# Kernel optimization log

Measured on AMD Instinct MI355X. Metric: run time of the kernel, lower is better.

The kernel has to match this reference:

```python
import jax, jax.numpy as jnp
import numpy as np

N_FACES = 40000
N_EDGES = 60000
NNZ = 3 * N_FACES  # 3 boundary edges per triangular face
IN_CH = 512
MID_CH = 512
OUT_CH = 512


def setup_inputs() -> dict:
    key = jax.random.key(0)
    k1, k2, k3 = jax.random.split(key, 3)
    x = jax.random.normal(k1, (N_FACES, IN_CH), dtype=jnp.float32)
    # xavier-uniform-ish scale with gain 1.414 as in TopoModelX Conv.reset_parameters
    W1 = jax.random.normal(k2, (IN_CH, MID_CH), dtype=jnp.float32) * (1.414 / np.sqrt(IN_CH))
    W2 = jax.random.normal(k3, (MID_CH, OUT_CH), dtype=jnp.float32) * (1.414 / np.sqrt(MID_CH))
    # COO incidence B2 [n_edges, n_faces]: face f -> edges (3f)%E,(3f+1)%E,(3f+2)%E
    i = jnp.arange(NNZ)
    face_idx = (i // 3).astype(jnp.int32)
    edge_idx = (i % N_EDGES).astype(jnp.int32)
    vals = jnp.ones((NNZ,), dtype=jnp.float32)
    return {"x": x, "W1": W1, "W2": W2, "edge_idx": edge_idx, "face_idx": face_idx, "vals": vals}


def _spmm(rows, cols, vals, x, n_rows):
    # y[r, :] = sum_{nnz with row r} vals * x[col, :]
    return jax.ops.segment_sum(vals[:, None] * x[cols], rows, num_segments=n_rows)


def reference(x, W1, W2, edge_idx, face_idx, vals):
    # row sums of B2 and B2^T for aggr_norm
    deg_e = jax.ops.segment_sum(vals, edge_idx, num_segments=N_EDGES)  # [n_edges]
    deg_f = jax.ops.segment_sum(vals, face_idx, num_segments=N_FACES)  # [n_faces]
    # conv level1: faces -> edges
    h = _spmm(edge_idx, face_idx, vals, x @ W1, N_EDGES)  # [n_edges, mid]
    h = jax.nn.sigmoid(h / deg_e[:, None])
    # conv level2: edges -> faces (transpose incidence)
    y = _spmm(face_idx, edge_idx, vals, h @ W2, N_FACES)  # [n_faces, out]
    return jax.nn.sigmoid(y / deg_f[:, None])
```

## Files before the change

### kernel.cpp

```cpp
#include <hip/hip_runtime.h>
#include <cstdint>

#define N_FACES_C 40000
#define N_EDGES_C 60000
#define CH        512

typedef __bf16 bf16_t;
typedef __bf16 bf16x8 __attribute__((ext_vector_type(8)));
typedef float  f32x4  __attribute__((ext_vector_type(4)));
static_assert(sizeof(bf16x8) == 16, "bf16x8 must be 16B");

__global__ void detect_dtype(const unsigned int* __restrict__ vals_bits, int* __restrict__ flag) {
  if (blockIdx.x == 0 && threadIdx.x == 0)
    *flag = (vals_bits[0] == 0x3F803F80u) ? 1 : 0;
}

__device__ __forceinline__ float load_val(const void* vals, int i, bool isbf16) {
  return isbf16 ? (float)((const bf16_t*)vals)[i] : ((const float*)vals)[i];
}

__device__ __forceinline__ float fast_sigmoid(float z) {
  float e = __builtin_amdgcn_exp2f(z * -1.44269504f);
  return __builtin_amdgcn_rcpf(1.0f + e);
}

__global__ void count_deg_kernel(const int* __restrict__ ei, const int* __restrict__ fi,
                                 const void* __restrict__ vals, int nnz,
                                 float* __restrict__ deg_e, float* __restrict__ deg_f,
                                 int* __restrict__ cnt_e, int* __restrict__ cnt_f,
                                 const int* __restrict__ flag) {
  int i = blockIdx.x * 256 + threadIdx.x;
  if (i >= nnz) return;
  bool isb = (*flag != 0);
  float v = load_val(vals, i, isb);
  int e = ei[i], f = fi[i];
  atomicAdd(&deg_e[e], v);
  atomicAdd(&deg_f[f], v);
  atomicAdd(&cnt_e[e], 1);
  atomicAdd(&cnt_f[f], 1);
}

__global__ void scan_part2(const int* __restrict__ cntE, int nE, int* __restrict__ bsumE,
                           const int* __restrict__ cntF, int nF, int* __restrict__ bsumF,
                           int nbE) {
  __shared__ int wsum[4];
  int bx = blockIdx.x;
  const int* cnt; int n; int* bsum; int b;
  if (bx < nbE) { cnt = cntE; n = nE; bsum = bsumE; b = bx; }
  else          { cnt = cntF; n = nF; bsum = bsumF; b = bx - nbE; }
  int t = threadIdx.x;
  int lane = t & 63, wave = t >> 6;
  int base = b * 1024 + t * 4;
  int s = 0;
#pragma unroll
  for (int k = 0; k < 4; ++k) {
    int idx = base + k;
    if (idx < n) s += cnt[idx];
  }
#pragma unroll
  for (int o = 32; o > 0; o >>= 1) s += __shfl_down(s, o);
  if (lane == 0) wsum[wave] = s;
  __syncthreads();
  if (t == 0) bsum[b] = wsum[0] + wsum[1] + wsum[2] + wsum[3];
}

__global__ void scan_bsums2(int* __restrict__ bsumE, int nbE, int* __restrict__ bsumF, int nbF) {
  int wave = threadIdx.x >> 6;
  int lane = threadIdx.x & 63;
  int* bsum = wave ? bsumF : bsumE;
  int nb    = wave ? nbF   : nbE;
  int orig = (lane < nb) ? bsum[lane] : 0;
  int v = orig;
#pragma unroll
  for (int o = 1; o < 64; o <<= 1) {
    int u = __shfl_up(v, o);
    if (lane >= o) v += u;
  }
  if (lane < nb) bsum[lane] = v - orig;
}

__global__ void scan_final2(const int* __restrict__ cntE, int nE, const int* __restrict__ bsumE,
                            int* __restrict__ ptrE, int* __restrict__ curE,
                            const int* __restrict__ cntF, int nF, const int* __restrict__ bsumF,
                            int* __restrict__ ptrF, int* __restrict__ curF, int nbE) {
  __shared__ int wsum[4];
  int bx = blockIdx.x;
  const int* cnt; int n; const int* bsum; int* ptr; int* cur; int b;
  if (bx < nbE) { cnt = cntE; n = nE; bsum = bsumE; ptr = ptrE; cur = curE; b = bx; }
  else          { cnt = cntF; n = nF; bsum = bsumF; ptr = ptrF; cur = curF; b = bx - nbE; }
  int t = threadIdx.x;
  int lane = t & 63, wave = t >> 6;
  int base = b * 1024 + t * 4;
  int c[4];
  int s = 0;
#pragma unroll
  for (int k = 0; k < 4; ++k) {
    int idx = base + k;
    c[k] = (idx < n) ? cnt[idx] : 0;
    s += c[k];
  }
  int v = s;
#pragma unroll
  for (int o = 1; o < 64; o <<= 1) {
    int u = __shfl_up(v, o);
    if (lane >= o) v += u;
  }
  if (lane == 63) wsum[wave] = v;
  __syncthreads();
  int woff = 0;
  for (int w = 0; w < wave; ++w) woff += wsum[w];
  int run = bsum[b] + woff + (v - s);
#pragma unroll
  for (int k = 0; k < 4; ++k) {
    int idx = base + k;
    if (idx < n) {
      ptr[idx] = run;
      cur[idx] = run;
      run += c[k];
      if (idx == n - 1) ptr[n] = run;
    }
  }
}

__global__ void csr_fill(const int* __restrict__ ei, const int* __restrict__ fi,
                         const void* __restrict__ vals, int nnz,
                         int* __restrict__ cur_e, int* __restrict__ col_e, float* __restrict__ val_e,
                         int* __restrict__ cur_f, int* __restrict__ col_f, float* __restrict__ val_f,
                         const int* __restrict__ flag) {
  int i = blockIdx.x * 256 + threadIdx.x;
  if (i >= nnz) return;
  bool isb = (*flag != 0);
  int e = ei[i], f = fi[i];
  float v = load_val(vals, i, isb);
  int p = atomicAdd(&cur_e[e], 1);
  col_e[p] = f; val_e[p] = v;
  int q = atomicAdd(&cur_f[f], 1);
  col_f[q] = e; val_f[q] = v;
}

__global__ void transposeW2(const void* __restrict__ W1, bf16_t* __restrict__ W1t,
                            const void* __restrict__ W2, bf16_t* __restrict__ W2t,
                            const int* __restrict__ flag) {
  __shared__ bf16_t tile[32][33];
  bool isb = (*flag != 0);
  const void* W = blockIdx.z ? W2 : W1;
  bf16_t*    Wt = blockIdx.z ? W2t : W1t;
  int bx = blockIdx.x * 32, by = blockIdx.y * 32;
  int tx = threadIdx.x, ty = threadIdx.y;
#pragma unroll
  for (int r = 0; r < 32; r += 8) {
    size_t idx = (size_t)(by + ty + r) * CH + bx + tx;
    tile[ty + r][tx] = isb ? ((const bf16_t*)W)[idx] : (bf16_t)((const float*)W)[idx];
  }
  __syncthreads();
#pragma unroll
  for (int r = 0; r < 32; r += 8)
    Wt[(size_t)(bx + ty + r) * CH + by + tx] = tile[tx][ty + r];
}

__global__ void spmm_div(const int* __restrict__ ptr, const int* __restrict__ cols,
                         const float* __restrict__ vals, const void* __restrict__ X,
                         const float* __restrict__ deg, bf16_t* __restrict__ Y,
                         int nRows, int nCols, int nnz,
                         const int* __restrict__ flag, int force_bf16) {
  int row = blockIdx.x * 4 + (threadIdx.x >> 6);
  if (row >= nRows) return;
  bool xb = force_bf16 || (*flag != 0);
  int lane = threadIdx.x & 63;
  int beg = ptr[row], end = ptr[row + 1];
  if (beg < 0) beg = 0;
  if (end > nnz) end = nnz;
  float acc[8];
#pragma unroll
  for (int t = 0; t < 8; ++t) acc[t] = 0.f;
  const int lofs = lane * 8;
  if (xb) {
    const bf16_t* Xb = (const bf16_t*)X;
    for (int p = beg; p < end; ++p) {
      int c = cols[p];
      if ((unsigned)c >= (unsigned)nCols) c = 0;
      float v = vals[p];
      bf16x8 xv = *(const bf16x8*)(Xb + (size_t)c * CH + lofs);
#pragma unroll
      for (int t = 0; t < 8; ++t) acc[t] += v * (float)xv[t];
    }
  } else {
    const float* Xf = (const float*)X;
    for (int p = beg; p < end; ++p) {
      int c = cols[p];
      if ((unsigned)c >= (unsigned)nCols) c = 0;
      float v = vals[p];
      const float* src = Xf + (size_t)c * CH + lofs;
      float4 a = *(const float4*)src;
      float4 b = *(const float4*)(src + 4);
      acc[0] += v * a.x; acc[1] += v * a.y; acc[2] += v * a.z; acc[3] += v * a.w;
      acc[4] += v * b.x; acc[5] += v * b.y; acc[6] += v * b.z; acc[7] += v * b.w;
    }
  }
  float d = deg[row];
  float invd = (d != 0.f) ? (1.0f / d) : 0.f;
  bf16x8 o;
#pragma unroll
  for (int t = 0; t < 8; ++t) o[t] = (bf16_t)(acc[t] * invd);
  *(bf16x8*)(Y + (size_t)row * CH + lofs) = o;
}

__global__ __launch_bounds__(256)
void gemm_sig(const bf16_t* __restrict__ A, const bf16_t* __restrict__ Bt,
              void* __restrict__ C, int M, int N, int K,
              const int* __restrict__ flag, int final_out) {
  __shared__ __align__(16) bf16_t As[128 * 64];
  __shared__ __align__(16) bf16_t Bs[128 * 64];
  const int tid  = threadIdx.x;
  const int lane = tid & 63;
  const int wave = tid >> 6;
  const int r0 = blockIdx.y * 128;
  const int c0 = blockIdx.x * 128;
  const int wr = (wave >> 1) * 64;
  const int wc = (wave & 1) * 64;
  const int q   = lane >> 4;
  const int l16 = lane & 15;
  const int srow_base = wave * 8 + (lane >> 3);
  const int sslot = lane & 7;

  f32x4 acc[4][4];
#pragma unroll
  for (int i = 0; i < 4; ++i)
#pragma unroll
    for (int j = 0; j < 4; ++j)
      acc[i][j] = (f32x4){0.f, 0.f, 0.f, 0.f};

  const int kTiles = K >> 6;
  for (int kt = 0; kt < kTiles; ++kt) {
    const int kb = kt * 64;
#pragma unroll
    for (int i = 0; i < 4; ++i) {
      const int lr = i * 32 + srow_base;
      const int gofs = (sslot ^ (lr & 7)) * 8;
      int ra = r0 + lr; if (ra > M - 1) ra = M - 1;
      const bf16_t* ga = A  + (size_t)ra * K + kb + gofs;
      const bf16_t* gb = Bt + (size_t)(c0 + lr) * K + kb + gofs;
      __builtin_amdgcn_global_load_lds((const __attribute__((address_space(1))) void*)ga,
                                       (__attribute__((address_space(3))) void*)(As + (i * 32 + wave * 8) * 64), 16, 0, 0);
      __builtin_amdgcn_global_load_lds((const __attribute__((address_space(1))) void*)gb,
                                       (__attribute__((address_space(3))) void*)(Bs + (i * 32 + wave * 8) * 64), 16, 0, 0);
    }
    __syncthreads();

#pragma unroll
    for (int kk = 0; kk < 2; ++kk) {
      const int slot = (kk * 4 + q) ^ (l16 & 7);
      const int ro = slot * 8;
      bf16x8 af[4], bfv[4];
#pragma unroll
      for (int i = 0; i < 4; ++i)
        af[i] = *(const bf16x8*)(As + (wr + i * 16 + l16) * 64 + ro);
#pragma unroll
      for (int j = 0; j < 4; ++j)
        bfv[j] = *(const bf16x8*)(Bs + (wc + j * 16 + l16) * 64 + ro);
#pragma unroll
      for (int i = 0; i < 4; ++i)
#pragma unroll
        for (int j = 0; j < 4; ++j)
          acc[i][j] = __builtin_amdgcn_mfma_f32_16x16x32_bf16(af[i], bfv[j], acc[i][j], 0, 0, 0);
    }
    __syncthreads();
  }

  const bool f32out = final_out && (*flag == 0);
#pragma unroll
  for (int i = 0; i < 4; ++i) {
#pragma unroll
    for (int r = 0; r < 4; ++r) {
      int row = r0 + wr + i * 16 + q * 4 + r;
      if (row < M) {
#pragma unroll
        for (int j = 0; j < 4; ++j) {
          int col = c0 + wc + j * 16 + l16;
          float s = fast_sigmoid(acc[i][j][r]);
          if (f32out) ((float*)C)[(size_t)row * N + col] = s;
          else        ((bf16_t*)C)[(size_t)row * N + col] = (bf16_t)s;
        }
      }
    }
  }
}

extern "C" void kernel_launch(void* const* d_in, const int* in_sizes, int n_in,
                              void* d_out, int out_size, void* d_ws, size_t ws_size,
                              hipStream_t stream) {
  const void* x    = d_in[0];
  const void* W1   = d_in[1];
  const void* W2   = d_in[2];
  const int*  ei   = (const int*)d_in[3];
  const int*  fi   = (const int*)d_in[4];
  const void* vals = d_in[5];
  const int nnz = in_sizes[3];

  char* ws = (char*)d_ws;
  size_t off = 0;
  auto alloc = [&](size_t bytes) -> void* {
    void* p = ws + off;
    off = (off + bytes + 511) & ~((size_t)511);
    return p;
  };
  bf16_t* s1g  = (bf16_t*)alloc((size_t)N_EDGES_C * CH * 2);
  bf16_t* h    = (bf16_t*)alloc((size_t)N_EDGES_C * CH * 2);
  bf16_t* w1t  = (bf16_t*)alloc((size_t)CH * CH * 2);
  bf16_t* w2t  = (bf16_t*)alloc((size_t)CH * CH * 2);
  float* deg_e = (float*)alloc((size_t)N_EDGES_C * 4);
  float* deg_f = (float*)alloc((size_t)N_FACES_C * 4);
  int*   cnt_e = (int*)alloc((size_t)N_EDGES_C * 4);
  int*   cnt_f = (int*)alloc((size_t)N_FACES_C * 4);
  size_t zero_bytes = (size_t)((char*)cnt_f + (size_t)N_FACES_C * 4 - (char*)deg_e);
  int*   ptr_e = (int*)alloc((size_t)(N_EDGES_C + 1) * 4);
  int*   ptr_f = (int*)alloc((size_t)(N_FACES_C + 1) * 4);
  int*   cur_e = (int*)alloc((size_t)N_EDGES_C * 4);
  int*   cur_f = (int*)alloc((size_t)N_FACES_C * 4);
  int*   col_e = (int*)alloc((size_t)nnz * 4);
  float* val_e = (float*)alloc((size_t)nnz * 4);
  int*   col_f = (int*)alloc((size_t)nnz * 4);
  float* val_f = (float*)alloc((size_t)nnz * 4);
  int*   bsumE = (int*)alloc(64 * 4);
  int*   bsumF = (int*)alloc(64 * 4);
  int*   flag  = (int*)alloc(4);
  bf16_t* s1 = s1g;
  bf16_t* g  = s1g;

  detect_dtype<<<1, 64, 0, stream>>>((const unsigned int*)vals, flag);
  hipMemsetAsync(deg_e, 0, zero_bytes, stream);
  count_deg_kernel<<<(nnz + 255) / 256, 256, 0, stream>>>(ei, fi, vals, nnz,
                                                          deg_e, deg_f, cnt_e, cnt_f, flag);

  int nbE = (N_EDGES_C + 1023) / 1024, nbF = (N_FACES_C + 1023) / 1024;
  scan_part2 <<<nbE + nbF, 256, 0, stream>>>(cnt_e, N_EDGES_C, bsumE, cnt_f, N_FACES_C, bsumF, nbE);
  scan_bsums2<<<1, 128, 0, stream>>>(bsumE, nbE, bsumF, nbF);
  scan_final2<<<nbE + nbF, 256, 0, stream>>>(cnt_e, N_EDGES_C, bsumE, ptr_e, cur_e,
                                             cnt_f, N_FACES_C, bsumF, ptr_f, cur_f, nbE);
  csr_fill<<<(nnz + 255) / 256, 256, 0, stream>>>(ei, fi, vals, nnz,
                                                  cur_e, col_e, val_e, cur_f, col_f, val_f, flag);

  transposeW2<<<dim3(16, 16, 2), dim3(32, 8), 0, stream>>>(W1, w1t, W2, w2t, flag);

  spmm_div<<<(N_EDGES_C + 3) / 4, 256, 0, stream>>>(ptr_e, col_e, val_e, x, deg_e, s1,
                                                    N_EDGES_C, N_FACES_C, nnz, flag, 0);
  gemm_sig<<<dim3(CH / 128, (N_EDGES_C + 127) / 128), 256, 0, stream>>>(s1, w1t, h,
                                                                        N_EDGES_C, CH, CH, flag, 0);
  spmm_div<<<(N_FACES_C + 3) / 4, 256, 0, stream>>>(ptr_f, col_f, val_f, h, deg_f, g,
                                                    N_FACES_C, N_EDGES_C, nnz, flag, 1);
  gemm_sig<<<dim3(CH / 128, (N_FACES_C + 127) / 128), 256, 0, stream>>>(g, w2t, d_out,
                                                                        N_FACES_C, CH, CH, flag, 1);
}
```

Baseline: 316.0 us.

## Reorder first conv to GEMM-then-SpMM and fuse second SpMM gather into GEMM

```diff
diff --git a/kernel.cpp b/kernel.cpp
--- a/kernel.cpp
+++ b/kernel.cpp
@@ -158,14 +158,12 @@
     Wt[(size_t)(bx + ty + r) * CH + by + tx] = tile[tx][ty + r];
 }
 
-__global__ void spmm_div(const int* __restrict__ ptr, const int* __restrict__ cols,
-                         const float* __restrict__ vals, const void* __restrict__ X,
+__global__ void spmm_sig(const int* __restrict__ ptr, const int* __restrict__ cols,
+                         const float* __restrict__ vals, const bf16_t* __restrict__ X,
                          const float* __restrict__ deg, bf16_t* __restrict__ Y,
-                         int nRows, int nCols, int nnz,
-                         const int* __restrict__ flag, int force_bf16) {
+                         int nRows, int nCols, int nnz) {
   int row = blockIdx.x * 4 + (threadIdx.x >> 6);
   if (row >= nRows) return;
-  bool xb = force_bf16 || (*flag != 0);
   int lane = threadIdx.x & 63;
   int beg = ptr[row], end = ptr[row + 1];
   if (beg < 0) beg = 0;
@@ -174,41 +172,25 @@
 #pragma unroll
   for (int t = 0; t < 8; ++t) acc[t] = 0.f;
   const int lofs = lane * 8;
-  if (xb) {
-    const bf16_t* Xb = (const bf16_t*)X;
-    for (int p = beg; p < end; ++p) {
-      int c = cols[p];
-      if ((unsigned)c >= (unsigned)nCols) c = 0;
-      float v = vals[p];
-      bf16x8 xv = *(const bf16x8*)(Xb + (size_t)c * CH + lofs);
-#pragma unroll
-      for (int t = 0; t < 8; ++t) acc[t] += v * (float)xv[t];
-    }
-  } else {
-    const float* Xf = (const float*)X;
-    for (int p = beg; p < end; ++p) {
-      int c = cols[p];
-      if ((unsigned)c >= (unsigned)nCols) c = 0;
-      float v = vals[p];
-      const float* src = Xf + (size_t)c * CH + lofs;
-      float4 a = *(const float4*)src;
-      float4 b = *(const float4*)(src + 4);
-      acc[0] += v * a.x; acc[1] += v * a.y; acc[2] += v * a.z; acc[3] += v * a.w;
-      acc[4] += v * b.x; acc[5] += v * b.y; acc[6] += v * b.z; acc[7] += v * b.w;
-    }
+  for (int p = beg; p < end; ++p) {
+    int c = cols[p];
+    if ((unsigned)c >= (unsigned)nCols) c = 0;
+    float v = vals[p];
+    bf16x8 xv = *(const bf16x8*)(X + (size_t)c * CH + lofs);
+#pragma unroll
+    for (int t = 0; t < 8; ++t) acc[t] += v * (float)xv[t];
   }
   float d = deg[row];
   float invd = (d != 0.f) ? (1.0f / d) : 0.f;
   bf16x8 o;
 #pragma unroll
-  for (int t = 0; t < 8; ++t) o[t] = (bf16_t)(acc[t] * invd);
+  for (int t = 0; t < 8; ++t) o[t] = (bf16_t)fast_sigmoid(acc[t] * invd);
   *(bf16x8*)(Y + (size_t)row * CH + lofs) = o;
 }
 
 __global__ __launch_bounds__(256)
-void gemm_sig(const bf16_t* __restrict__ A, const bf16_t* __restrict__ Bt,
-              void* __restrict__ C, int M, int N, int K,
-              const int* __restrict__ flag, int final_out) {
+void gemm_xw(const void* __restrict__ A, const bf16_t* __restrict__ Bt,
+             bf16_t* __restrict__ C, int M, const int* __restrict__ flag) {
   __shared__ __align__(16) bf16_t As[128 * 64];
   __shared__ __align__(16) bf16_t Bs[128 * 64];
   const int tid  = threadIdx.x;
@@ -222,6 +204,7 @@
   const int l16 = lane & 15;
   const int srow_base = wave * 8 + (lane >> 3);
   const int sslot = lane & 7;
+  const bool ab = (*flag != 0);
 
   f32x4 acc[4][4];
 #pragma unroll
@@ -230,20 +213,37 @@
     for (int j = 0; j < 4; ++j)
       acc[i][j] = (f32x4){0.f, 0.f, 0.f, 0.f};
 
-  const int kTiles = K >> 6;
-  for (int kt = 0; kt < kTiles; ++kt) {
+  for (int kt = 0; kt < 8; ++kt) {
     const int kb = kt * 64;
-#pragma unroll
-    for (int i = 0; i < 4; ++i) {
-      const int lr = i * 32 + srow_base;
-      const int gofs = (sslot ^ (lr & 7)) * 8;
-      int ra = r0 + lr; if (ra > M - 1) ra = M - 1;
-      const bf16_t* ga = A  + (size_t)ra * K + kb + gofs;
-      const bf16_t* gb = Bt + (size_t)(c0 + lr) * K + kb + gofs;
-      __builtin_amdgcn_global_load_lds((const __attribute__((address_space(1))) void*)ga,
-                                       (__attribute__((address_space(3))) void*)(As + (i * 32 + wave * 8) * 64), 16, 0, 0);
-      __builtin_amdgcn_global_load_lds((const __attribute__((address_space(1))) void*)gb,
-                                       (__attribute__((address_space(3))) void*)(Bs + (i * 32 + wave * 8) * 64), 16, 0, 0);
+    if (ab) {
+      const bf16_t* Ab = (const bf16_t*)A;
+#pragma unroll
+      for (int i = 0; i < 4; ++i) {
+        const int lr = i * 32 + srow_base;
+        const int gofs = (sslot ^ (lr & 7)) * 8;
+        int ra = r0 + lr; if (ra > M - 1) ra = M - 1;
+        __builtin_amdgcn_global_load_lds((const __attribute__((address_space(1))) void*)(Ab + (size_t)ra * CH + kb + gofs),
+                                         (__attribute__((address_space(3))) void*)(As + (i * 32 + wave * 8) * 64), 16, 0, 0);
+        __builtin_amdgcn_global_load_lds((const __attribute__((address_space(1))) void*)(Bt + (size_t)(c0 + lr) * CH + kb + gofs),
+                                         (__attribute__((address_space(3))) void*)(Bs + (i * 32 + wave * 8) * 64), 16, 0, 0);
+      }
+    } else {
+      const float* Af = (const float*)A;
+#pragma unroll
+      for (int i = 0; i < 4; ++i) {
+        const int lr = i * 32 + srow_base;
+        const int gofs = (sslot ^ (lr & 7)) * 8;
+        int ra = r0 + lr; if (ra > M - 1) ra = M - 1;
+        const float* src = Af + (size_t)ra * CH + kb + gofs;
+        float4 a = *(const float4*)src;
+        float4 b = *(const float4*)(src + 4);
+        bf16x8 v;
+        v[0] = (bf16_t)a.x; v[1] = (bf16_t)a.y; v[2] = (bf16_t)a.z; v[3] = (bf16_t)a.w;
+        v[4] = (bf16_t)b.x; v[5] = (bf16_t)b.y; v[6] = (bf16_t)b.z; v[7] = (bf16_t)b.w;
+        *(bf16x8*)(As + lr * 64 + sslot * 8) = v;
+        __builtin_amdgcn_global_load_lds((const __attribute__((address_space(1))) void*)(Bt + (size_t)(c0 + lr) * CH + kb + gofs),
+                                         (__attribute__((address_space(3))) void*)(Bs + (i * 32 + wave * 8) * 64), 16, 0, 0);
+      }
     }
     __syncthreads();
 
@@ -267,7 +267,6 @@
     __syncthreads();
   }
 
-  const bool f32out = final_out && (*flag == 0);
 #pragma unroll
   for (int i = 0; i < 4; ++i) {
 #pragma unroll
@@ -277,9 +276,139 @@
 #pragma unroll
         for (int j = 0; j < 4; ++j) {
           int col = c0 + wc + j * 16 + l16;
+          C[(size_t)row * CH + col] = (bf16_t)acc[i][j][r];
+        }
+      }
+    }
+  }
+}
+
+__global__ __launch_bounds__(256)
+void gemm_gather_sig(const int* __restrict__ ptrR, const int* __restrict__ colsR,
+                     const float* __restrict__ valsR, const bf16_t* __restrict__ H,
+                     const float* __restrict__ deg, const bf16_t* __restrict__ Bt,
+                     void* __restrict__ C, int M, int nColsH, int nnz,
+                     const int* __restrict__ flag) {
+  __shared__ __align__(16) bf16_t As[128 * 64];
+  __shared__ __align__(16) bf16_t Bs[128 * 64];
+  const int tid  = threadIdx.x;
+  const int lane = tid & 63;
+  const int wave = tid >> 6;
+  const int r0 = blockIdx.y * 128;
+  const int c0 = blockIdx.x * 128;
+  const int wr = (wave >> 1) * 64;
+  const int wc = (wave & 1) * 64;
+  const int q   = lane >> 4;
+  const int l16 = lane & 15;
+  const int srow_base = wave * 8 + (lane >> 3);
+  const int sslot = lane & 7;
+
+  int   beg_[4], cnt_[4];
+  float invd_[4];
+  int   gc[4][4];
+  float gv[4][4];
+#pragma unroll
+  for (int i = 0; i < 4; ++i) {
+    const int lr = i * 32 + srow_base;
+    int ra = r0 + lr; if (ra > M - 1) ra = M - 1;
+    int b = ptrR[ra], e = ptrR[ra + 1];
+    if (b < 0) b = 0;
+    if (e > nnz) e = nnz;
+    if (e < b) e = b;
+    int n = e - b;
+    beg_[i] = b; cnt_[i] = n;
+    float d = deg[ra];
+    invd_[i] = (d != 0.f) ? (1.0f / d) : 0.f;
+    int c0v = 0;
+    if (n > 0) {
+      c0v = colsR[b];
+      if ((unsigned)c0v >= (unsigned)nColsH) c0v = 0;
+    }
+#pragma unroll
+    for (int p = 0; p < 4; ++p) {
+      int c = c0v; float v = 0.f;
+      if (p < n) {
+        c = colsR[b + p];
+        if ((unsigned)c >= (unsigned)nColsH) c = 0;
+        v = valsR[b + p];
+      }
+      gc[i][p] = c; gv[i][p] = v;
+    }
+  }
+
+  f32x4 acc[4][4];
+#pragma unroll
+  for (int i = 0; i < 4; ++i)
+#pragma unroll
+    for (int j = 0; j < 4; ++j)
+      acc[i][j] = (f32x4){0.f, 0.f, 0.f, 0.f};
+
+  for (int kt = 0; kt < 8; ++kt) {
+    const int kb = kt * 64;
+#pragma unroll
+    for (int i = 0; i < 4; ++i) {
+      const int lr = i * 32 + srow_base;
+      const int gofs = (sslot ^ (lr & 7)) * 8;
+      float a8[8];
+#pragma unroll
+      for (int t = 0; t < 8; ++t) a8[t] = 0.f;
+#pragma unroll
+      for (int p = 0; p < 4; ++p) {
+        bf16x8 hv = *(const bf16x8*)(H + (size_t)gc[i][p] * CH + kb + gofs);
+        float v = gv[i][p];
+#pragma unroll
+        for (int t = 0; t < 8; ++t) a8[t] += v * (float)hv[t];
+      }
+      for (int p = 4; p < cnt_[i]; ++p) {
+        int c = colsR[beg_[i] + p];
+        if ((unsigned)c >= (unsigned)nColsH) c = 0;
+        float v = valsR[beg_[i] + p];
+        bf16x8 hv = *(const bf16x8*)(H + (size_t)c * CH + kb + gofs);
+#pragma unroll
+        for (int t = 0; t < 8; ++t) a8[t] += v * (float)hv[t];
+      }
+      bf16x8 av;
+#pragma unroll
+      for (int t = 0; t < 8; ++t) av[t] = (bf16_t)(a8[t] * invd_[i]);
+      *(bf16x8*)(As + lr * 64 + sslot * 8) = av;
+      __builtin_amdgcn_global_load_lds((const __attribute__((address_space(1))) void*)(Bt + (size_t)(c0 + lr) * CH + kb + gofs),
+                                       (__attribute__((address_space(3))) void*)(Bs + (i * 32 + wave * 8) * 64), 16, 0, 0);
+    }
+    __syncthreads();
+
+#pragma unroll
+    for (int kk = 0; kk < 2; ++kk) {
+      const int slot = (kk * 4 + q) ^ (l16 & 7);
+      const int ro = slot * 8;
+      bf16x8 af[4], bfv[4];
+#pragma unroll
+      for (int i = 0; i < 4; ++i)
+        af[i] = *(const bf16x8*)(As + (wr + i * 16 + l16) * 64 + ro);
+#pragma unroll
+      for (int j = 0; j < 4; ++j)
+        bfv[j] = *(const bf16x8*)(Bs + (wc + j * 16 + l16) * 64 + ro);
+#pragma unroll
+      for (int i = 0; i < 4; ++i)
+#pragma unroll
+        for (int j = 0; j < 4; ++j)
+          acc[i][j] = __builtin_amdgcn_mfma_f32_16x16x32_bf16(af[i], bfv[j], acc[i][j], 0, 0, 0);
+    }
+    __syncthreads();
+  }
+
+  const bool f32out = (*flag == 0);
+#pragma unroll
+  for (int i = 0; i < 4; ++i) {
+#pragma unroll
+    for (int r = 0; r < 4; ++r) {
+      int row = r0 + wr + i * 16 + q * 4 + r;
+      if (row < M) {
+#pragma unroll
+        for (int j = 0; j < 4; ++j) {
+          int col = c0 + wc + j * 16 + l16;
           float s = fast_sigmoid(acc[i][j][r]);
-          if (f32out) ((float*)C)[(size_t)row * N + col] = s;
-          else        ((bf16_t*)C)[(size_t)row * N + col] = (bf16_t)s;
+          if (f32out) ((float*)C)[(size_t)row * CH + col] = s;
+          else        ((bf16_t*)C)[(size_t)row * CH + col] = (bf16_t)s;
         }
       }
     }
@@ -304,7 +433,7 @@
     off = (off + bytes + 511) & ~((size_t)511);
     return p;
   };
-  bf16_t* s1g  = (bf16_t*)alloc((size_t)N_EDGES_C * CH * 2);
+  bf16_t* t    = (bf16_t*)alloc((size_t)N_FACES_C * CH * 2);
   bf16_t* h    = (bf16_t*)alloc((size_t)N_EDGES_C * CH * 2);
   bf16_t* w1t  = (bf16_t*)alloc((size_t)CH * CH * 2);
   bf16_t* w2t  = (bf16_t*)alloc((size_t)CH * CH * 2);
@@ -324,8 +453,6 @@
   int*   bsumE = (int*)alloc(64 * 4);
   int*   bsumF = (int*)alloc(64 * 4);
   int*   flag  = (int*)alloc(4);
-  bf16_t* s1 = s1g;
-  bf16_t* g  = s1g;
 
   detect_dtype<<<1, 64, 0, stream>>>((const unsigned int*)vals, flag);
   hipMemsetAsync(deg_e, 0, zero_bytes, stream);
@@ -342,12 +469,9 @@
 
   transposeW2<<<dim3(16, 16, 2), dim3(32, 8), 0, stream>>>(W1, w1t, W2, w2t, flag);
 
-  spmm_div<<<(N_EDGES_C + 3) / 4, 256, 0, stream>>>(ptr_e, col_e, val_e, x, deg_e, s1,
-                                                    N_EDGES_C, N_FACES_C, nnz, flag, 0);
-  gemm_sig<<<dim3(CH / 128, (N_EDGES_C + 127) / 128), 256, 0, stream>>>(s1, w1t, h,
-                                                                        N_EDGES_C, CH, CH, flag, 0);
-  spmm_div<<<(N_FACES_C + 3) / 4, 256, 0, stream>>>(ptr_f, col_f, val_f, h, deg_f, g,
-                                                    N_FACES_C, N_EDGES_C, nnz, flag, 1);
-  gemm_sig<<<dim3(CH / 128, (N_FACES_C + 127) / 128), 256, 0, stream>>>(g, w2t, d_out,
-                                                                        N_FACES_C, CH, CH, flag, 1);
-}
+  gemm_xw<<<dim3(CH / 128, (N_FACES_C + 127) / 128), 256, 0, stream>>>(x, w1t, t, N_FACES_C, flag);
+  spmm_sig<<<(N_EDGES_C + 3) / 4, 256, 0, stream>>>(ptr_e, col_e, val_e, t, deg_e, h,
+                                                    N_EDGES_C, N_FACES_C, nnz);
+  gemm_gather_sig<<<dim3(CH / 128, (N_FACES_C + 127) / 128), 256, 0, stream>>>(
+      ptr_f, col_f, val_f, h, deg_f, w2t, d_out, N_FACES_C, N_EDGES_C, nnz, flag);
+}
```

New measurement: 402.5 us. +27.4%, slower.

## Reorder GEMM before first SpMM to run GEMM on fewer face rows

Applied to the files above, without the earlier changes.

```diff
diff --git a/kernel.cpp b/kernel.cpp
--- a/kernel.cpp
+++ b/kernel.cpp
@@ -158,57 +158,82 @@
     Wt[(size_t)(bx + ty + r) * CH + by + tx] = tile[tx][ty + r];
 }
 
-__global__ void spmm_div(const int* __restrict__ ptr, const int* __restrict__ cols,
-                         const float* __restrict__ vals, const void* __restrict__ X,
+__global__ void cvt_x(const float* __restrict__ X, bf16_t* __restrict__ Xb,
+                      const int* __restrict__ flag) {
+  if (*flag != 0) return;
+  size_t i = (size_t)blockIdx.x * 256 + threadIdx.x;
+  const float4* src = (const float4*)X + i * 2;
+  float4 a = src[0];
+  float4 b = src[1];
+  bf16x8 v;
+  v[0] = (bf16_t)a.x; v[1] = (bf16_t)a.y; v[2] = (bf16_t)a.z; v[3] = (bf16_t)a.w;
+  v[4] = (bf16_t)b.x; v[5] = (bf16_t)b.y; v[6] = (bf16_t)b.z; v[7] = (bf16_t)b.w;
+  *((bf16x8*)Xb + i) = v;
+}
+
+template <int SIG>
+__global__ void spmm_row(const int* __restrict__ ptr, const int* __restrict__ cols,
+                         const float* __restrict__ vals, const bf16_t* __restrict__ X,
                          const float* __restrict__ deg, bf16_t* __restrict__ Y,
-                         int nRows, int nCols, int nnz,
-                         const int* __restrict__ flag, int force_bf16) {
+                         int nRows, int nCols, int nnz) {
   int row = blockIdx.x * 4 + (threadIdx.x >> 6);
   if (row >= nRows) return;
-  bool xb = force_bf16 || (*flag != 0);
   int lane = threadIdx.x & 63;
   int beg = ptr[row], end = ptr[row + 1];
   if (beg < 0) beg = 0;
   if (end > nnz) end = nnz;
+  int n = end - beg; if (n < 0) n = 0;
+  const int lofs = lane * 8;
+  int cfirst = 0;
+  if (n > 0) {
+    cfirst = cols[beg];
+    if ((unsigned)cfirst >= (unsigned)nCols) cfirst = 0;
+  }
+  int   c4[4]; float v4[4];
+#pragma unroll
+  for (int p = 0; p < 4; ++p) {
+    int c = cfirst; float v = 0.f;
+    if (p < n) {
+      c = cols[beg + p];
+      if ((unsigned)c >= (unsigned)nCols) c = 0;
+      v = vals[beg + p];
+    }
+    c4[p] = c; v4[p] = v;
+  }
+  bf16x8 xv[4];
+#pragma unroll
+  for (int p = 0; p < 4; ++p)
+    xv[p] = *(const bf16x8*)(X + (size_t)c4[p] * CH + lofs);
   float acc[8];
 #pragma unroll
   for (int t = 0; t < 8; ++t) acc[t] = 0.f;
-  const int lofs = lane * 8;
-  if (xb) {
-    const bf16_t* Xb = (const bf16_t*)X;
-    for (int p = beg; p < end; ++p) {
-      int c = cols[p];
-      if ((unsigned)c >= (unsigned)nCols) c = 0;
-      float v = vals[p];
-      bf16x8 xv = *(const bf16x8*)(Xb + (size_t)c * CH + lofs);
-#pragma unroll
-      for (int t = 0; t < 8; ++t) acc[t] += v * (float)xv[t];
-    }
-  } else {
-    const float* Xf = (const float*)X;
-    for (int p = beg; p < end; ++p) {
-      int c = cols[p];
-      if ((unsigned)c >= (unsigned)nCols) c = 0;
-      float v = vals[p];
-      const float* src = Xf + (size_t)c * CH + lofs;
-      float4 a = *(const float4*)src;
-      float4 b = *(const float4*)(src + 4);
-      acc[0] += v * a.x; acc[1] += v * a.y; acc[2] += v * a.z; acc[3] += v * a.w;
-      acc[4] += v * b.x; acc[5] += v * b.y; acc[6] += v * b.z; acc[7] += v * b.w;
-    }
+#pragma unroll
+  for (int p = 0; p < 4; ++p)
+#pragma unroll
+    for (int t = 0; t < 8; ++t) acc[t] += v4[p] * (float)xv[p][t];
+  for (int p = beg + 4; p < end; ++p) {
+    int c = cols[p];
+    if ((unsigned)c >= (unsigned)nCols) c = 0;
+    float v = vals[p];
+    bf16x8 q = *(const bf16x8*)(X + (size_t)c * CH + lofs);
+#pragma unroll
+    for (int t = 0; t < 8; ++t) acc[t] += v * (float)q[t];
   }
   float d = deg[row];
   float invd = (d != 0.f) ? (1.0f / d) : 0.f;
   bf16x8 o;
 #pragma unroll
-  for (int t = 0; t < 8; ++t) o[t] = (bf16_t)(acc[t] * invd);
+  for (int t = 0; t < 8; ++t) {
+    float z = acc[t] * invd;
+    o[t] = (bf16_t)(SIG ? fast_sigmoid(z) : z);
+  }
   *(bf16x8*)(Y + (size_t)row * CH + lofs) = o;
 }
 
 __global__ __launch_bounds__(256)
-void gemm_sig(const bf16_t* __restrict__ A, const bf16_t* __restrict__ Bt,
-              void* __restrict__ C, int M, int N, int K,
-              const int* __restrict__ flag, int final_out) {
+void gemm_tile(const bf16_t* __restrict__ Aorig, const bf16_t* __restrict__ Acvt,
+               const bf16_t* __restrict__ Bt, void* __restrict__ C, int M,
+               const int* __restrict__ flag, int do_sig, int final_out) {
   __shared__ __align__(16) bf16_t As[128 * 64];
   __shared__ __align__(16) bf16_t Bs[128 * 64];
   const int tid  = threadIdx.x;
@@ -222,6 +247,7 @@
   const int l16 = lane & 15;
   const int srow_base = wave * 8 + (lane >> 3);
   const int sslot = lane & 7;
+  const bf16_t* A = (*flag != 0) ? Aorig : Acvt;
 
   f32x4 acc[4][4];
 #pragma unroll
@@ -230,16 +256,15 @@
     for (int j = 0; j < 4; ++j)
       acc[i][j] = (f32x4){0.f, 0.f, 0.f, 0.f};
 
-  const int kTiles = K >> 6;
-  for (int kt = 0; kt < kTiles; ++kt) {
+  for (int kt = 0; kt < 8; ++kt) {
     const int kb = kt * 64;
 #pragma unroll
     for (int i = 0; i < 4; ++i) {
       const int lr = i * 32 + srow_base;
       const int gofs = (sslot ^ (lr & 7)) * 8;
       int ra = r0 + lr; if (ra > M - 1) ra = M - 1;
-      const bf16_t* ga = A  + (size_t)ra * K + kb + gofs;
-      const bf16_t* gb = Bt + (size_t)(c0 + lr) * K + kb + gofs;
+      const bf16_t* ga = A  + (size_t)ra * CH + kb + gofs;
+      const bf16_t* gb = Bt + (size_t)(c0 + lr) * CH + kb + gofs;
       __builtin_amdgcn_global_load_lds((const __attribute__((address_space(1))) void*)ga,
                                        (__attribute__((address_space(3))) void*)(As + (i * 32 + wave * 8) * 64), 16, 0, 0);
       __builtin_amdgcn_global_load_lds((const __attribute__((address_space(1))) void*)gb,
@@ -277,9 +302,10 @@
 #pragma unroll
         for (int j = 0; j < 4; ++j) {
           int col = c0 + wc + j * 16 + l16;
-          float s = fast_sigmoid(acc[i][j][r]);
-          if (f32out) ((float*)C)[(size_t)row * N + col] = s;
-          else        ((bf16_t*)C)[(size_t)row * N + col] = (bf16_t)s;
+          float s = acc[i][j][r];
+          if (do_sig) s = fast_sigmoid(s);
+          if (f32out) ((float*)C)[(size_t)row * CH + col] = s;
+          else        ((bf16_t*)C)[(size_t)row * CH + col] = (bf16_t)s;
         }
       }
     }
@@ -304,8 +330,10 @@
     off = (off + bytes + 511) & ~((size_t)511);
     return p;
   };
-  bf16_t* s1g  = (bf16_t*)alloc((size_t)N_EDGES_C * CH * 2);
+  bf16_t* t    = (bf16_t*)alloc((size_t)N_FACES_C * CH * 2);
   bf16_t* h    = (bf16_t*)alloc((size_t)N_EDGES_C * CH * 2);
+  bf16_t* g    = (bf16_t*)alloc((size_t)N_FACES_C * CH * 2);
+  bf16_t* xb   = g;
   bf16_t* w1t  = (bf16_t*)alloc((size_t)CH * CH * 2);
   bf16_t* w2t  = (bf16_t*)alloc((size_t)CH * CH * 2);
   float* deg_e = (float*)alloc((size_t)N_EDGES_C * 4);
@@ -324,8 +352,6 @@
   int*   bsumE = (int*)alloc(64 * 4);
   int*   bsumF = (int*)alloc(64 * 4);
   int*   flag  = (int*)alloc(4);
-  bf16_t* s1 = s1g;
-  bf16_t* g  = s1g;
 
   detect_dtype<<<1, 64, 0, stream>>>((const unsigned int*)vals, flag);
   hipMemsetAsync(deg_e, 0, zero_bytes, stream);
@@ -342,12 +368,14 @@
 
   transposeW2<<<dim3(16, 16, 2), dim3(32, 8), 0, stream>>>(W1, w1t, W2, w2t, flag);
 
-  spmm_div<<<(N_EDGES_C + 3) / 4, 256, 0, stream>>>(ptr_e, col_e, val_e, x, deg_e, s1,
-                                                    N_EDGES_C, N_FACES_C, nnz, flag, 0);
-  gemm_sig<<<dim3(CH / 128, (N_EDGES_C + 127) / 128), 256, 0, stream>>>(s1, w1t, h,
-                                                                        N_EDGES_C, CH, CH, flag, 0);
-  spmm_div<<<(N_FACES_C + 3) / 4, 256, 0, stream>>>(ptr_f, col_f, val_f, h, deg_f, g,
-                                                    N_FACES_C, N_EDGES_C, nnz, flag, 1);
-  gemm_sig<<<dim3(CH / 128, (N_FACES_C + 127) / 128), 256, 0, stream>>>(g, w2t, d_out,
-                                                                        N_FACES_C, CH, CH, flag, 1);
-}
+  cvt_x<<<(N_FACES_C * CH / 8 + 255) / 256, 256, 0, stream>>>((const float*)x, xb, flag);
+
+  gemm_tile<<<dim3(CH / 128, (N_FACES_C + 127) / 128), 256, 0, stream>>>(
+      (const bf16_t*)x, xb, w1t, t, N_FACES_C, flag, 0, 0);
+  spmm_row<1><<<(N_EDGES_C + 3) / 4, 256, 0, stream>>>(ptr_e, col_e, val_e, t, deg_e, h,
+                                                       N_EDGES_C, N_FACES_C, nnz);
+  spmm_row<0><<<(N_FACES_C + 3) / 4, 256, 0, stream>>>(ptr_f, col_f, val_f, h, deg_f, g,
+                                                       N_FACES_C, N_EDGES_C, nnz);
+  gemm_tile<<<dim3(CH / 128, (N_FACES_C + 127) / 128), 256, 0, stream>>>(
+      g, g, w2t, d_out, N_FACES_C, flag, 1, 1);
+}
```

Result: slower. 324.2 us (+2.6%).
